# Optimization experiments

Measured on AMD Instinct MI355X. Metric: run time of the kernel, lower is better.

## Reference

```python
import jax, jax.numpy as jnp
import numpy as np

C = 256       # in_channels
IC = 128      # inter_channels = C // 2
G = 4         # num_group
D = IC // G   # per-group channels = 32
B, H, W_ = 4, 56, 56
EPS = 1e-5


def conv1x1(x, w, b=None):
    # x: (B,Cin,H,W), w: (Cout,Cin)
    y = jnp.einsum('bchw,oc->bohw', x, w)
    if b is not None:
        y = y + b[None, :, None, None]
    return y


def bn(x, scale, bias, mean, var):
    inv = scale / jnp.sqrt(var + EPS)
    return x * inv[None, :, None, None] + (bias - mean * inv)[None, :, None, None]


def setup_inputs():
    key = jax.random.key(0)
    ks = jax.random.split(key, 16)
    r = lambda k, shape, s=0.05: jax.random.normal(k, shape, jnp.float32) * s
    C4 = C // 4
    return {
        'x': jax.random.normal(ks[0], (B, C, H, W_), jnp.float32),
        'g_w': r(ks[1], (IC, C)), 'g_b': r(ks[2], (IC,)),
        'theta_w': r(ks[3], (IC, C)), 'theta_b': r(ks[4], (IC,)),
        'phi_w': r(ks[5], (IC, C)), 'phi_b': r(ks[6], (IC,)),
        'W_w': r(ks[7], (C, IC)), 'W_b': r(ks[8], (C,)),
        'bnW_scale': jnp.ones((C,)), 'bnW_bias': jnp.zeros((C,)),
        'bnW_mean': jnp.zeros((C,)), 'bnW_var': jnp.ones((C,)),
        'ff1_w': r(ks[9], (C4, C)),
        'ffbn1_scale': jnp.ones((C4,)), 'ffbn1_bias': jnp.zeros((C4,)),
        'ffbn1_mean': jnp.zeros((C4,)), 'ffbn1_var': jnp.ones((C4,)),
        'ff2_w': r(ks[10], (C4, C4, 3, 3)),
        'ffbn2_scale': jnp.ones((C4,)), 'ffbn2_bias': jnp.zeros((C4,)),
        'ffbn2_mean': jnp.zeros((C4,)), 'ffbn2_var': jnp.ones((C4,)),
        'ff3_w': r(ks[11], (C, C4)),
        'ffbn3_scale': jnp.ones((C,)), 'ffbn3_bias': jnp.zeros((C,)),
        'ffbn3_mean': jnp.zeros((C,)), 'ffbn3_var': jnp.ones((C,)),
    }


def reference(x, g_w, g_b, theta_w, theta_b, phi_w, phi_b, W_w, W_b,
              bnW_scale, bnW_bias, bnW_mean, bnW_var,
              ff1_w, ffbn1_scale, ffbn1_bias, ffbn1_mean, ffbn1_var,
              ff2_w, ffbn2_scale, ffbn2_bias, ffbn2_mean, ffbn2_var,
              ff3_w, ffbn3_scale, ffbn3_bias, ffbn3_mean, ffbn3_var):
    b, c, h, w = x.shape
    n = h * w
    # grouped non-local attention: channels split into G groups of D
    gx = conv1x1(x, g_w, g_b).reshape(b, G, D, n)       # (B,G,D,N)
    tx = conv1x1(x, theta_w, theta_b).reshape(b, G, D, n)
    px = conv1x1(x, phi_w, phi_b).reshape(b, G, D, n)
    f = jnp.einsum('bgdn,bgdm->bgnm', tx, px)           # (B,G,N,N) scores
    attn = jax.nn.softmax(f, axis=-1)                   # softmax over keys (torch dim=2 on (b,N,N))
    yy = jnp.einsum('bgnm,bgdm->bgdn', attn, gx)        # (B,G,D,N)
    y_out = yy.reshape(b, IC, h, w)
    W_y = bn(conv1x1(y_out, W_w, W_b), bnW_scale, bnW_bias, bnW_mean, bnW_var)
    z = jax.nn.relu(W_y + x)
    # FPNFFConv bottleneck FFN (BN in eval mode)
    o = jax.nn.relu(bn(conv1x1(z, ff1_w), ffbn1_scale, ffbn1_bias, ffbn1_mean, ffbn1_var))
    o = jax.lax.conv_general_dilated(o, ff2_w, (1, 1), 'SAME',
                                     dimension_numbers=('NCHW', 'OIHW', 'NCHW'))
    o = jax.nn.relu(bn(o, ffbn2_scale, ffbn2_bias, ffbn2_mean, ffbn2_var))
    o = bn(conv1x1(o, ff3_w), ffbn3_scale, ffbn3_bias, ffbn3_mean, ffbn3_var)
    return jax.nn.relu(o + z)
```

## Files before the change

kernel.cpp:

```cpp
#include <hip/hip_runtime.h>
#include <hip/hip_bf16.h>

#define NPIX 3136
#define BB 4
#define LOG2E 1.4426950408889634f

typedef unsigned short u16;
typedef __bf16 bf16x8 __attribute__((ext_vector_type(8)));
typedef float f32x4 __attribute__((ext_vector_type(4)));

__device__ __forceinline__ float b2f(u16 u) {
  union { unsigned u; float f; } c; c.u = ((unsigned)u) << 16; return c.f;
}
__device__ __forceinline__ u16 f2b(float f) {
  __hip_bfloat16 h = __float2bfloat16(f);
  return *reinterpret_cast<u16*>(&h);
}
__device__ __forceinline__ unsigned pk2(float a, float b) {
  return (unsigned)f2b(a) | ((unsigned)f2b(b) << 16);
}
__device__ __forceinline__ f32x4 mfma(bf16x8 a, bf16x8 b, f32x4 c) {
  return __builtin_amdgcn_mfma_f32_16x16x32_bf16(a, b, c, 0, 0, 0);
}

template<int NSTEP, int NOT>
__device__ __forceinline__ void mf_gemm2(const u16* __restrict__ A0,
                                         const u16* __restrict__ A1,
                                         const u16* __restrict__ Brow, int sB,
                                         int lq, f32x4* acc) {
#pragma unroll
  for (int s = 0; s < NSTEP; ++s) {
    bf16x8 bf[NOT];
#pragma unroll
    for (int ot = 0; ot < NOT; ++ot)
      bf[ot] = *(const bf16x8*)(Brow + (size_t)ot * 16 * sB + s * 32 + lq * 8);
    bf16x8 a0 = *(const bf16x8*)(A0 + s * 32 + lq * 8);
    bf16x8 a1 = *(const bf16x8*)(A1 + s * 32 + lq * 8);
#pragma unroll
    for (int ot = 0; ot < NOT; ++ot) {
      acc[ot] = mfma(a0, bf[ot], acc[ot]);
      acc[NOT + ot] = mfma(a1, bf[ot], acc[NOT + ot]);
    }
  }
}

__global__ __launch_bounds__(256) void prep_w(
    const float* __restrict__ gw, const float* __restrict__ tw,
    const float* __restrict__ pw, const float* __restrict__ Ww,
    const float* __restrict__ f1w, const float* __restrict__ f2w,
    const float* __restrict__ f3w,
    u16* __restrict__ gwb, u16* __restrict__ twb, u16* __restrict__ pwb,
    u16* __restrict__ Wwb, u16* __restrict__ f1b, u16* __restrict__ f3b,
    u16* __restrict__ f2p) {
  for (int i = blockIdx.x * 256 + threadIdx.x; i < 200704; i += gridDim.x * 256) {
    int j = i;
    if (j < 32768) { gwb[j] = f2b(gw[j]); continue; } j -= 32768;
    if (j < 32768) { twb[j] = f2b(tw[j] * LOG2E); continue; } j -= 32768;
    if (j < 32768) { pwb[j] = f2b(pw[j]); continue; } j -= 32768;
    if (j < 32768) { Wwb[j] = f2b(Ww[j]); continue; } j -= 32768;
    if (j < 16384) { f1b[j] = f2b(f1w[j]); continue; } j -= 16384;
    if (j < 16384) { f3b[j] = f2b(f3w[j]); continue; } j -= 16384;
    int t = j >> 12, rem = j & 4095, co = rem >> 6, ci = rem & 63;
    f2p[j] = f2b(f2w[(co * 64 + ci) * 9 + t]);
  }
}

__global__ __launch_bounds__(256) void prep_x(const float* __restrict__ x,
                                              u16* __restrict__ xt) {
  __shared__ u16 sT[64 * 65];
  const int b = blockIdx.z, c0 = blockIdx.y * 64, n0 = blockIdx.x * 64;
  const int t = threadIdx.x;
#pragma unroll
  for (int cc = 0; cc < 4; ++cc) {
    int c = cc * 16 + (t >> 4), n4 = (t & 15) * 4;
    float4 v = *(const float4*)(x + ((size_t)(b * 256 + c0 + c)) * NPIX + n0 + n4);
    sT[c * 65 + n4 + 0] = f2b(v.x);
    sT[c * 65 + n4 + 1] = f2b(v.y);
    sT[c * 65 + n4 + 2] = f2b(v.z);
    sT[c * 65 + n4 + 3] = f2b(v.w);
  }
  __syncthreads();
#pragma unroll
  for (int nn = 0; nn < 4; ++nn) {
    int n = nn * 16 + (t >> 4), c4 = (t & 15) * 4;
    uint2 s;
    s.x = (unsigned)sT[(c4 + 0) * 65 + n] | ((unsigned)sT[(c4 + 1) * 65 + n] << 16);
    s.y = (unsigned)sT[(c4 + 2) * 65 + n] | ((unsigned)sT[(c4 + 3) * 65 + n] << 16);
    *(uint2*)(xt + ((size_t)b * NPIX + n0 + n) * 256 + c0 + c4) = s;
  }
}

__global__ __launch_bounds__(256) void proj_kernel(
    const u16* __restrict__ xt,
    const u16* __restrict__ gwb, const u16* __restrict__ twb, const u16* __restrict__ pwb,
    const float* __restrict__ gb, const float* __restrict__ tb, const float* __restrict__ pb,
    u16* __restrict__ gx, u16* __restrict__ Tq, u16* __restrict__ Pk) {
  const int b = blockIdx.z, oc = blockIdx.y, nb = blockIdx.x * 128;
  const int sec = oc >> 1, rbase = (oc & 1) * 64;
  const u16* wsel = sec == 0 ? gwb : (sec == 1 ? twb : pwb);
  const float* bsel = sec == 0 ? gb : (sec == 1 ? tb : pb);
  const int wv = threadIdx.x >> 6, lane = threadIdx.x & 63;
  const int lr = lane & 15, lq = lane >> 4;
  const int nrow0 = nb + wv * 32, nrow1 = nrow0 + 16;
  const int r0 = nrow0 + lr < NPIX ? nrow0 + lr : NPIX - 1;
  const int r1 = nrow1 + lr < NPIX ? nrow1 + lr : NPIX - 1;
  f32x4 acc[8] = {};
  mf_gemm2<8, 4>(xt + ((size_t)b * NPIX + r0) * 256,
                 xt + ((size_t)b * NPIX + r1) * 256,
                 wsel + (size_t)(rbase + lr) * 256, 256, lq, acc);
#pragma unroll
  for (int t = 0; t < 2; ++t) {
    const int qn = (t ? nrow1 : nrow0) + lq * 4;
    if (qn >= NPIX) continue;
#pragma unroll
    for (int ot = 0; ot < 4; ++ot) {
      const f32x4 a = acc[t * 4 + ot];
      const int o = rbase + ot * 16 + lr;
      float bias = bsel[o];
      if (sec == 1) bias *= LOG2E;
      if (sec == 0) {
        uint2 s;
        s.x = pk2(a[0] + bias, a[1] + bias);
        s.y = pk2(a[2] + bias, a[3] + bias);
        *(uint2*)(gx + ((size_t)b * 128 + o) * NPIX + qn) = s;
      } else {
        const int g = o >> 5, dl = o & 31;
        u16* dst = sec == 1 ? Tq : Pk;
        size_t base = (size_t)(b * 4 + g) * NPIX;
#pragma unroll
        for (int r = 0; r < 4; ++r)
          dst[(base + qn + r) * 32 + dl] = f2b(a[r] + bias);
      }
    }
  }
}

__global__ __launch_bounds__(256) void attn_kernel(
    const u16* __restrict__ Tq, const u16* __restrict__ Pk,
    const u16* __restrict__ gx, u16* __restrict__ OPb, float* __restrict__ LP) {
  __shared__ __align__(16) u16 Plds[4][32][40];
  const int bid = blockIdx.x;
  const int ks = bid / 400, rem = bid % 400;
  const int bg = rem / 25, qblk = rem % 25;
  const int b = bg >> 2, g = bg & 3;
  const int wave = threadIdx.x >> 6, lane = threadIdx.x & 63;
  const int lr = lane & 15, lq = lane >> 4;
  const int qbase = qblk * 128 + wave * 32;
  const int kc0 = ks * 448;
  const u16* Qp = Tq + (size_t)bg * NPIX * 32;
  const u16* Kp = Pk + (size_t)bg * NPIX * 32;
  const u16* Vp = gx + ((size_t)b * 128 + g * 32) * NPIX;

  bf16x8 qf[2];
#pragma unroll
  for (int qi = 0; qi < 2; ++qi) {
    int row = qbase + qi * 16 + lr;
    row = row < NPIX ? row : NPIX - 1;
    qf[qi] = *(const bf16x8*)(Qp + (size_t)row * 32 + lq * 8);
  }
  const f32x4 z4 = {0.f, 0.f, 0.f, 0.f};
  f32x4 O[2][2], Lf[2];
#pragma unroll
  for (int qi = 0; qi < 2; ++qi) { O[qi][0] = z4; O[qi][1] = z4; Lf[qi] = z4; }
  bf16x8 onef;
#pragma unroll
  for (int j = 0; j < 8; ++j) onef[j] = (__bf16)1.0f;

#pragma unroll 1
  for (int kc = kc0; kc < kc0 + 448; kc += 32) {
    bf16x8 kf0 = *(const bf16x8*)(Kp + (size_t)(kc + lr) * 32 + lq * 8);
    bf16x8 kf1 = *(const bf16x8*)(Kp + (size_t)(kc + 16 + lr) * 32 + lq * 8);
    f32x4 S[2][2];
    S[0][0] = mfma(qf[0], kf0, z4);
    S[0][1] = mfma(qf[0], kf1, z4);
    S[1][0] = mfma(qf[1], kf0, z4);
    S[1][1] = mfma(qf[1], kf1, z4);
#pragma unroll
    for (int qi = 0; qi < 2; ++qi)
#pragma unroll
      for (int kt = 0; kt < 2; ++kt)
#pragma unroll
        for (int r = 0; r < 4; ++r) {
          unsigned u = __builtin_bit_cast(unsigned, __builtin_exp2f(S[qi][kt][r]));
          Plds[wave][qi * 16 + lq * 4 + r][kt * 16 + lr] = (u16)(u >> 16);
        }
    bf16x8 pf0 = *(const bf16x8*)(&Plds[wave][lr][lq * 8]);
    bf16x8 pf1 = *(const bf16x8*)(&Plds[wave][16 + lr][lq * 8]);
    bf16x8 vf0 = *(const bf16x8*)(Vp + (size_t)lr * NPIX + kc + lq * 8);
    bf16x8 vf1 = *(const bf16x8*)(Vp + (size_t)(16 + lr) * NPIX + kc + lq * 8);
    O[0][0] = mfma(pf0, vf0, O[0][0]);
    O[0][1] = mfma(pf0, vf1, O[0][1]);
    O[1][0] = mfma(pf1, vf0, O[1][0]);
    O[1][1] = mfma(pf1, vf1, O[1][1]);
    Lf[0] = mfma(pf0, onef, Lf[0]);
    Lf[1] = mfma(pf1, onef, Lf[1]);
  }
  const size_t sbase = (size_t)(ks * 16 + bg) * NPIX;
#pragma unroll
  for (int qi = 0; qi < 2; ++qi) {
#pragma unroll
    for (int r = 0; r < 4; ++r) {
      int qrow = qbase + qi * 16 + lq * 4 + r;
      if (qrow < NPIX) {
        size_t ob = (sbase + qrow) * 32;
        OPb[ob + lr] = f2b(O[qi][0][r]);
        OPb[ob + 16 + lr] = f2b(O[qi][1][r]);
        if (lr == 0) LP[sbase + qrow] = Lf[qi][r];
      }
    }
  }
}

__global__ __launch_bounds__(256) void combine_kernel(
    const u16* __restrict__ OPb, const float* __restrict__ LP,
    u16* __restrict__ yt) {
  const int bg = blockIdx.y, b = bg >> 2, g = bg & 3;
  const int t = threadIdx.x;
  const int n = blockIdx.x * 64 + (t >> 2);
  const int dseg = (t & 3) * 8;
  float a[8] = {};
  float l = 0.f;
#pragma unroll
  for (int ks = 0; ks < 7; ++ks) {
    const u16* src = OPb + ((size_t)(ks * 16 + bg) * NPIX + n) * 32 + dseg;
    uint4 v = *(const uint4*)src;
    const unsigned* vp = (const unsigned*)&v;
#pragma unroll
    for (int k = 0; k < 4; ++k) {
      a[2 * k] += b2f((u16)vp[k]);
      a[2 * k + 1] += b2f((u16)(vp[k] >> 16));
    }
    l += LP[(size_t)(ks * 16 + bg) * NPIX + n];
  }
  float inv = 1.0f / l;
  uint4 s;
  s.x = pk2(a[0] * inv, a[1] * inv);
  s.y = pk2(a[2] * inv, a[3] * inv);
  s.z = pk2(a[4] * inv, a[5] * inv);
  s.w = pk2(a[6] * inv, a[7] * inv);
  *(uint4*)(yt + ((size_t)b * NPIX + n) * 128 + g * 32 + dseg) = s;
}

__global__ __launch_bounds__(256) void wz_kernel(
    const u16* __restrict__ yt, const u16* __restrict__ Wwb, const float* __restrict__ Wb,
    const float* __restrict__ sc, const float* __restrict__ bi,
    const float* __restrict__ mu, const float* __restrict__ var,
    const float* __restrict__ x, u16* __restrict__ zt) {
  const int b = blockIdx.z, oc = blockIdx.y, nb = blockIdx.x * 128;
  const int wv = threadIdx.x >> 6, lane = threadIdx.x & 63;
  const int lr = lane & 15, lq = lane >> 4;
  const int nrow0 = nb + wv * 32, nrow1 = nrow0 + 16;
  const int r0 = nrow0 + lr < NPIX ? nrow0 + lr : NPIX - 1;
  const int r1 = nrow1 + lr < NPIX ? nrow1 + lr : NPIX - 1;
  f32x4 acc[8] = {};
  mf_gemm2<4, 4>(yt + ((size_t)b * NPIX + r0) * 128,
                 yt + ((size_t)b * NPIX + r1) * 128,
                 Wwb + (size_t)(oc * 64 + lr) * 128, 128, lq, acc);
#pragma unroll
  for (int t = 0; t < 2; ++t) {
    const int qn = (t ? nrow1 : nrow0) + lq * 4;
    if (qn >= NPIX) continue;
#pragma unroll
    for (int ot = 0; ot < 4; ++ot) {
      const f32x4 a = acc[t * 4 + ot];
      const int o = oc * 64 + ot * 16 + lr;
      float inv = sc[o] * rsqrtf(var[o] + 1e-5f);
      float off = bi[o] - mu[o] * inv + Wb[o] * inv;
      float4 xr = *(const float4*)(x + ((size_t)b * 256 + o) * NPIX + qn);
      float xv[4] = {xr.x, xr.y, xr.z, xr.w};
#pragma unroll
      for (int r = 0; r < 4; ++r) {
        float v = fmaxf(a[r] * inv + off + xv[r], 0.f);
        zt[((size_t)b * NPIX + qn + r) * 256 + o] = f2b(v);
      }
    }
  }
}

__global__ __launch_bounds__(256) void ff1_kernel(
    const u16* __restrict__ zt, const u16* __restrict__ f1b,
    const float* __restrict__ sc, const float* __restrict__ bi,
    const float* __restrict__ mu, const float* __restrict__ var,
    u16* __restrict__ o1t) {
  const int b = blockIdx.z, oc = blockIdx.y, nb = blockIdx.x * 128;
  const int wv = threadIdx.x >> 6, lane = threadIdx.x & 63;
  const int lr = lane & 15, lq = lane >> 4;
  const int nrow0 = nb + wv * 32, nrow1 = nrow0 + 16;
  const int r0 = nrow0 + lr < NPIX ? nrow0 + lr : NPIX - 1;
  const int r1 = nrow1 + lr < NPIX ? nrow1 + lr : NPIX - 1;
  f32x4 acc[4] = {};
  mf_gemm2<8, 2>(zt + ((size_t)b * NPIX + r0) * 256,
                 zt + ((size_t)b * NPIX + r1) * 256,
                 f1b + (size_t)(oc * 32 + lr) * 256, 256, lq, acc);
#pragma unroll
  for (int t = 0; t < 2; ++t) {
    const int qn = (t ? nrow1 : nrow0) + lq * 4;
    if (qn >= NPIX) continue;
#pragma unroll
    for (int ot = 0; ot < 2; ++ot) {
      const f32x4 a = acc[t * 2 + ot];
      const int o = oc * 32 + ot * 16 + lr;
      float inv = sc[o] * rsqrtf(var[o] + 1e-5f);
      float off = bi[o] - mu[o] * inv;
#pragma unroll
      for (int r = 0; r < 4; ++r) {
        float v = fmaxf(a[r] * inv + off, 0.f);
        o1t[((size_t)b * NPIX + qn + r) * 64 + o] = f2b(v);
      }
    }
  }
}

__global__ __launch_bounds__(256) void ff2_kernel(
    const u16* __restrict__ o1t, const u16* __restrict__ f2p,
    const float* __restrict__ sc, const float* __restrict__ bi,
    const float* __restrict__ mu, const float* __restrict__ var,
    u16* __restrict__ o2t) {
  const int b = blockIdx.z, oc = blockIdx.y, nb = blockIdx.x * 128;
  const int wv = threadIdx.x >> 6, lane = threadIdx.x & 63;
  const int lr = lane & 15, lq = lane >> 4;
  const int n0 = nb + wv * 32 + lr, n1 = n0 + 16;
  const int h0 = n0 / 56, w0 = n0 % 56;
  const int h1 = n1 / 56, w1 = n1 % 56;
  f32x4 acc[4] = {};
#pragma unroll
  for (int t = 0; t < 9; ++t) {
    const int dh = t / 3 - 1, dw = t % 3 - 1;
    const bool v0 = (h0 + dh) >= 0 && (h0 + dh) < 56 && (w0 + dw) >= 0 && (w0 + dw) < 56;
    const bool v1 = (h1 + dh) >= 0 && (h1 + dh) < 56 && (w1 + dw) >= 0 && (w1 + dw) < 56;
    const u16* A0 = o1t + ((size_t)b * NPIX + n0 + dh * 56 + dw) * 64;
    const u16* A1 = o1t + ((size_t)b * NPIX + n1 + dh * 56 + dw) * 64;
    const u16* Br = f2p + (size_t)t * 4096 + (size_t)(oc * 32 + lr) * 64;
#pragma unroll
    for (int k2 = 0; k2 < 2; ++k2) {
      bf16x8 bf0 = *(const bf16x8*)(Br + k2 * 32 + lq * 8);
      bf16x8 bf1 = *(const bf16x8*)(Br + (size_t)16 * 64 + k2 * 32 + lq * 8);
      bf16x8 a0 = {}, a1 = {};
      if (v0) a0 = *(const bf16x8*)(A0 + k2 * 32 + lq * 8);
      if (v1) a1 = *(const bf16x8*)(A1 + k2 * 32 + lq * 8);
      acc[0] = mfma(a0, bf0, acc[0]);
      acc[1] = mfma(a0, bf1, acc[1]);
      acc[2] = mfma(a1, bf0, acc[2]);
      acc[3] = mfma(a1, bf1, acc[3]);
    }
  }
  const int nrow0 = nb + wv * 32;
#pragma unroll
  for (int t = 0; t < 2; ++t) {
    const int qn = nrow0 + t * 16 + lq * 4;
    if (qn >= NPIX) continue;
#pragma unroll
    for (int ot = 0; ot < 2; ++ot) {
      const f32x4 a = acc[t * 2 + ot];
      const int o = oc * 32 + ot * 16 + lr;
      float inv = sc[o] * rsqrtf(var[o] + 1e-5f);
      float off = bi[o] - mu[o] * inv;
#pragma unroll
      for (int r = 0; r < 4; ++r) {
        float v = fmaxf(a[r] * inv + off, 0.f);
        o2t[((size_t)b * NPIX + qn + r) * 64 + o] = f2b(v);
      }
    }
  }
}

__global__ __launch_bounds__(256) void ff3_kernel(
    const u16* __restrict__ o2t, const u16* __restrict__ f3b,
    const float* __restrict__ sc, const float* __restrict__ bi,
    const float* __restrict__ mu, const float* __restrict__ var,
    const u16* __restrict__ zt, float* __restrict__ out) {
  const int b = blockIdx.z, oc = blockIdx.y, nb = blockIdx.x * 128;
  const int wv = threadIdx.x >> 6, lane = threadIdx.x & 63;
  const int lr = lane & 15, lq = lane >> 4;
  const int nrow0 = nb + wv * 32, nrow1 = nrow0 + 16;
  const int r0 = nrow0 + lr < NPIX ? nrow0 + lr : NPIX - 1;
  const int r1 = nrow1 + lr < NPIX ? nrow1 + lr : NPIX - 1;
  f32x4 acc[8] = {};
  mf_gemm2<2, 4>(o2t + ((size_t)b * NPIX + r0) * 64,
                 o2t + ((size_t)b * NPIX + r1) * 64,
                 f3b + (size_t)(oc * 64 + lr) * 64, 64, lq, acc);
#pragma unroll
  for (int t = 0; t < 2; ++t) {
    const int qn = (t ? nrow1 : nrow0) + lq * 4;
    if (qn >= NPIX) continue;
#pragma unroll
    for (int ot = 0; ot < 4; ++ot) {
      const f32x4 a = acc[t * 4 + ot];
      const int o = oc * 64 + ot * 16 + lr;
      float inv = sc[o] * rsqrtf(var[o] + 1e-5f);
      float off = bi[o] - mu[o] * inv;
      float4 s;
      float* sv = (float*)&s;
#pragma unroll
      for (int r = 0; r < 4; ++r) {
        float zres = b2f(zt[((size_t)b * NPIX + qn + r) * 256 + o]);
        sv[r] = fmaxf(a[r] * inv + off + zres, 0.f);
      }
      *(float4*)(out + ((size_t)b * 256 + o) * NPIX + qn) = s;
    }
  }
}

extern "C" void kernel_launch(void* const* d_in, const int* in_sizes, int n_in,
                              void* d_out, int out_size, void* d_ws, size_t ws_size,
                              hipStream_t stream) {
  const float* x    = (const float*)d_in[0];
  const float* gw   = (const float*)d_in[1];
  const float* gb   = (const float*)d_in[2];
  const float* tw   = (const float*)d_in[3];
  const float* tb   = (const float*)d_in[4];
  const float* pw   = (const float*)d_in[5];
  const float* pb   = (const float*)d_in[6];
  const float* Ww   = (const float*)d_in[7];
  const float* Wb   = (const float*)d_in[8];
  const float* bnWs = (const float*)d_in[9];
  const float* bnWb = (const float*)d_in[10];
  const float* bnWm = (const float*)d_in[11];
  const float* bnWv = (const float*)d_in[12];
  const float* f1w  = (const float*)d_in[13];
  const float* b1s  = (const float*)d_in[14];
  const float* b1b  = (const float*)d_in[15];
  const float* b1m  = (const float*)d_in[16];
  const float* b1v  = (const float*)d_in[17];
  const float* f2w  = (const float*)d_in[18];
  const float* b2s  = (const float*)d_in[19];
  const float* b2b  = (const float*)d_in[20];
  const float* b2m  = (const float*)d_in[21];
  const float* b2v  = (const float*)d_in[22];
  const float* f3w  = (const float*)d_in[23];
  const float* b3s  = (const float*)d_in[24];
  const float* b3b  = (const float*)d_in[25];
  const float* b3m  = (const float*)d_in[26];
  const float* b3v  = (const float*)d_in[27];
  float* out = (float*)d_out;

  u16* p = (u16*)d_ws;
  u16* xt  = p; p += (size_t)BB * NPIX * 256;
  u16* gwb = p; p += 128 * 256;
  u16* twb = p; p += 128 * 256;
  u16* pwb = p; p += 128 * 256;
  u16* Wwb = p; p += 256 * 128;
  u16* f1b = p; p += 64 * 256;
  u16* f3b = p; p += 256 * 64;
  u16* f2p = p; p += 9 * 64 * 64;
  u16* Tq  = p; p += (size_t)16 * NPIX * 32;
  u16* Pk  = p; p += (size_t)16 * NPIX * 32;
  u16* gx  = p; p += (size_t)BB * 128 * NPIX;
  u16* yt  = p; p += (size_t)BB * NPIX * 128;
  u16* OPb = p; p += (size_t)7 * 16 * NPIX * 32;
  float* LP = (float*)p; p += (size_t)7 * 16 * NPIX * 2;
  u16* zt  = p; p += (size_t)BB * NPIX * 256;
  u16* o1t = p; p += (size_t)BB * NPIX * 64;
  u16* o2t = p; p += (size_t)BB * NPIX * 64;

  prep_w<<<dim3(196), 256, 0, stream>>>(gw, tw, pw, Ww, f1w, f2w, f3w,
                                        gwb, twb, pwb, Wwb, f1b, f3b, f2p);
  prep_x<<<dim3(49, 4, BB), 256, 0, stream>>>(x, xt);
  proj_kernel<<<dim3(25, 6, BB), 256, 0, stream>>>(xt, gwb, twb, pwb, gb, tb, pb,
                                                   gx, Tq, Pk);
  attn_kernel<<<dim3(2800), 256, 0, stream>>>(Tq, Pk, gx, OPb, LP);
  combine_kernel<<<dim3(49, 16), 256, 0, stream>>>(OPb, LP, yt);
  wz_kernel<<<dim3(25, 4, BB), 256, 0, stream>>>(yt, Wwb, Wb, bnWs, bnWb, bnWm, bnWv,
                                                 x, zt);
  ff1_kernel<<<dim3(25, 2, BB), 256, 0, stream>>>(zt, f1b, b1s, b1b, b1m, b1v, o1t);
  ff2_kernel<<<dim3(25, 2, BB), 256, 0, stream>>>(o1t, f2p, b2s, b2b, b2m, b2v, o2t);
  ff3_kernel<<<dim3(25, 4, BB), 256, 0, stream>>>(o2t, f3b, b3s, b3b, b3m, b3v, zt, out);
}
```

Before: 250.9 us.

## Fuse x transpose into projection and split-K combine into W conv

```diff
diff --git a/kernel.cpp b/kernel.cpp
--- a/kernel.cpp
+++ b/kernel.cpp
@@ -65,71 +65,62 @@
   }
 }
 
-__global__ __launch_bounds__(256) void prep_x(const float* __restrict__ x,
-                                              u16* __restrict__ xt) {
-  __shared__ u16 sT[64 * 65];
-  const int b = blockIdx.z, c0 = blockIdx.y * 64, n0 = blockIdx.x * 64;
-  const int t = threadIdx.x;
-#pragma unroll
-  for (int cc = 0; cc < 4; ++cc) {
-    int c = cc * 16 + (t >> 4), n4 = (t & 15) * 4;
-    float4 v = *(const float4*)(x + ((size_t)(b * 256 + c0 + c)) * NPIX + n0 + n4);
-    sT[c * 65 + n4 + 0] = f2b(v.x);
-    sT[c * 65 + n4 + 1] = f2b(v.y);
-    sT[c * 65 + n4 + 2] = f2b(v.z);
-    sT[c * 65 + n4 + 3] = f2b(v.w);
-  }
-  __syncthreads();
-#pragma unroll
-  for (int nn = 0; nn < 4; ++nn) {
-    int n = nn * 16 + (t >> 4), c4 = (t & 15) * 4;
-    uint2 s;
-    s.x = (unsigned)sT[(c4 + 0) * 65 + n] | ((unsigned)sT[(c4 + 1) * 65 + n] << 16);
-    s.y = (unsigned)sT[(c4 + 2) * 65 + n] | ((unsigned)sT[(c4 + 3) * 65 + n] << 16);
-    *(uint2*)(xt + ((size_t)b * NPIX + n0 + n) * 256 + c0 + c4) = s;
-  }
-}
-
 __global__ __launch_bounds__(256) void proj_kernel(
-    const u16* __restrict__ xt,
+    const float* __restrict__ x,
     const u16* __restrict__ gwb, const u16* __restrict__ twb, const u16* __restrict__ pwb,
     const float* __restrict__ gb, const float* __restrict__ tb, const float* __restrict__ pb,
     u16* __restrict__ gx, u16* __restrict__ Tq, u16* __restrict__ Pk) {
-  const int b = blockIdx.z, oc = blockIdx.y, nb = blockIdx.x * 128;
-  const int sec = oc >> 1, rbase = (oc & 1) * 64;
-  const u16* wsel = sec == 0 ? gwb : (sec == 1 ? twb : pwb);
-  const float* bsel = sec == 0 ? gb : (sec == 1 ? tb : pb);
-  const int wv = threadIdx.x >> 6, lane = threadIdx.x & 63;
-  const int lr = lane & 15, lq = lane >> 4;
-  const int nrow0 = nb + wv * 32, nrow1 = nrow0 + 16;
-  const int r0 = nrow0 + lr < NPIX ? nrow0 + lr : NPIX - 1;
-  const int r1 = nrow1 + lr < NPIX ? nrow1 + lr : NPIX - 1;
-  f32x4 acc[8] = {};
-  mf_gemm2<8, 4>(xt + ((size_t)b * NPIX + r0) * 256,
-                 xt + ((size_t)b * NPIX + r1) * 256,
-                 wsel + (size_t)(rbase + lr) * 256, 256, lq, acc);
-#pragma unroll
-  for (int t = 0; t < 2; ++t) {
-    const int qn = (t ? nrow1 : nrow0) + lq * 4;
-    if (qn >= NPIX) continue;
+  __shared__ __align__(16) u16 sA[64 * 264];
+  const int b = blockIdx.y, nb = blockIdx.x * 64;
+  const int tid = threadIdx.x;
+  const int cb16 = tid >> 4, jj = tid & 15;
+#pragma unroll 4
+  for (int cb = 0; cb < 16; ++cb) {
+    int c = cb * 16 + cb16;
+    float4 v = *(const float4*)(x + ((size_t)(b * 256 + c)) * NPIX + nb + jj * 4);
+    int n0 = jj * 4;
+    sA[(n0 + 0) * 264 + c] = f2b(v.x);
+    sA[(n0 + 1) * 264 + c] = f2b(v.y);
+    sA[(n0 + 2) * 264 + c] = f2b(v.z);
+    sA[(n0 + 3) * 264 + c] = f2b(v.w);
+  }
+  __syncthreads();
+  const int wv = tid >> 6, lane = tid & 63;
+  const int lr = lane & 15, lq = lane >> 4;
+  const int nrow = nb + wv * 16;
+#pragma unroll 1
+  for (int sec = 0; sec < 6; ++sec) {
+    const int st = sec >> 1, rbase = (sec & 1) * 64;
+    const u16* wsel = st == 0 ? gwb : (st == 1 ? twb : pwb);
+    const float* bsel = st == 0 ? gb : (st == 1 ? tb : pb);
+    f32x4 acc[4] = {};
+#pragma unroll
+    for (int s = 0; s < 8; ++s) {
+      bf16x8 af = *(const bf16x8*)(sA + (wv * 16 + lr) * 264 + s * 32 + lq * 8);
+#pragma unroll
+      for (int ot = 0; ot < 4; ++ot) {
+        bf16x8 bf = *(const bf16x8*)(wsel + (size_t)(rbase + ot * 16 + lr) * 256 + s * 32 + lq * 8);
+        acc[ot] = mfma(af, bf, acc[ot]);
+      }
+    }
+    const int qn = nrow + lq * 4;
 #pragma unroll
     for (int ot = 0; ot < 4; ++ot) {
-      const f32x4 a = acc[t * 4 + ot];
       const int o = rbase + ot * 16 + lr;
       float bias = bsel[o];
-      if (sec == 1) bias *= LOG2E;
-      if (sec == 0) {
-        uint2 s;
-        s.x = pk2(a[0] + bias, a[1] + bias);
-        s.y = pk2(a[2] + bias, a[3] + bias);
-        *(uint2*)(gx + ((size_t)b * 128 + o) * NPIX + qn) = s;
+      if (st == 1) bias *= LOG2E;
+      if (st == 0) {
+        uint2 s2;
+        s2.x = pk2(acc[ot][0] + bias, acc[ot][1] + bias);
+        s2.y = pk2(acc[ot][2] + bias, acc[ot][3] + bias);
+        *(uint2*)(gx + ((size_t)b * 128 + o) * NPIX + qn) = s2;
       } else {
         const int g = o >> 5, dl = o & 31;
-        u16* dst = sec == 1 ? Tq : Pk;
+        u16* dst = st == 1 ? Tq : Pk;
         size_t base = (size_t)(b * 4 + g) * NPIX;
 #pragma unroll
         for (int r = 0; r < 4; ++r)
-          dst[(base + qn + r) * 32 + dl] = f2b(a[r] + bias);
+          dst[(base + qn + r) * 32 + dl] = f2b(acc[ot][r] + bias);
       }
     }
   }
@@ -211,68 +202,58 @@
   }
 }
 
-__global__ __launch_bounds__(256) void combine_kernel(
+__global__ __launch_bounds__(256) void wz_kernel(
     const u16* __restrict__ OPb, const float* __restrict__ LP,
-    u16* __restrict__ yt) {
-  const int bg = blockIdx.y, b = bg >> 2, g = bg & 3;
-  const int t = threadIdx.x;
-  const int n = blockIdx.x * 64 + (t >> 2);
-  const int dseg = (t & 3) * 8;
-  float a[8] = {};
-  float l = 0.f;
-#pragma unroll
-  for (int ks = 0; ks < 7; ++ks) {
-    const u16* src = OPb + ((size_t)(ks * 16 + bg) * NPIX + n) * 32 + dseg;
-    uint4 v = *(const uint4*)src;
-    const unsigned* vp = (const unsigned*)&v;
-#pragma unroll
-    for (int k = 0; k < 4; ++k) {
-      a[2 * k] += b2f((u16)vp[k]);
-      a[2 * k + 1] += b2f((u16)(vp[k] >> 16));
-    }
-    l += LP[(size_t)(ks * 16 + bg) * NPIX + n];
-  }
-  float inv = 1.0f / l;
-  uint4 s;
-  s.x = pk2(a[0] * inv, a[1] * inv);
-  s.y = pk2(a[2] * inv, a[3] * inv);
-  s.z = pk2(a[4] * inv, a[5] * inv);
-  s.w = pk2(a[6] * inv, a[7] * inv);
-  *(uint4*)(yt + ((size_t)b * NPIX + n) * 128 + g * 32 + dseg) = s;
-}
-
-__global__ __launch_bounds__(256) void wz_kernel(
-    const u16* __restrict__ yt, const u16* __restrict__ Wwb, const float* __restrict__ Wb,
+    const u16* __restrict__ Wwb, const float* __restrict__ Wb,
     const float* __restrict__ sc, const float* __restrict__ bi,
     const float* __restrict__ mu, const float* __restrict__ var,
     const float* __restrict__ x, u16* __restrict__ zt) {
-  const int b = blockIdx.z, oc = blockIdx.y, nb = blockIdx.x * 128;
-  const int wv = threadIdx.x >> 6, lane = threadIdx.x & 63;
-  const int lr = lane & 15, lq = lane >> 4;
-  const int nrow0 = nb + wv * 32, nrow1 = nrow0 + 16;
-  const int r0 = nrow0 + lr < NPIX ? nrow0 + lr : NPIX - 1;
-  const int r1 = nrow1 + lr < NPIX ? nrow1 + lr : NPIX - 1;
-  f32x4 acc[8] = {};
-  mf_gemm2<4, 4>(yt + ((size_t)b * NPIX + r0) * 128,
-                 yt + ((size_t)b * NPIX + r1) * 128,
-                 Wwb + (size_t)(oc * 64 + lr) * 128, 128, lq, acc);
-#pragma unroll
-  for (int t = 0; t < 2; ++t) {
-    const int qn = (t ? nrow1 : nrow0) + lq * 4;
-    if (qn >= NPIX) continue;
-#pragma unroll
-    for (int ot = 0; ot < 4; ++ot) {
-      const f32x4 a = acc[t * 4 + ot];
-      const int o = oc * 64 + ot * 16 + lr;
-      float inv = sc[o] * rsqrtf(var[o] + 1e-5f);
-      float off = bi[o] - mu[o] * inv + Wb[o] * inv;
-      float4 xr = *(const float4*)(x + ((size_t)b * 256 + o) * NPIX + qn);
-      float xv[4] = {xr.x, xr.y, xr.z, xr.w};
-#pragma unroll
-      for (int r = 0; r < 4; ++r) {
-        float v = fmaxf(a[r] * inv + off + xv[r], 0.f);
-        zt[((size_t)b * NPIX + qn + r) * 256 + o] = f2b(v);
-      }
+  __shared__ float Ls[4][64];
+  const int b = blockIdx.z, oc = blockIdx.y, nb = blockIdx.x * 64;
+  const int tid = threadIdx.x;
+  {
+    int g = tid >> 6, row = tid & 63;
+    float l = 0.f;
+#pragma unroll
+    for (int ks = 0; ks < 7; ++ks)
+      l += LP[(size_t)(ks * 16 + b * 4 + g) * NPIX + nb + row];
+    Ls[g][row] = 1.0f / l;
+  }
+  __syncthreads();
+  const int wv = tid >> 6, lane = tid & 63;
+  const int lr = lane & 15, lq = lane >> 4;
+  const int nrow = nb + wv * 16;
+  f32x4 acc[4][4] = {};
+#pragma unroll
+  for (int g = 0; g < 4; ++g) {
+    bf16x8 bf[4];
+#pragma unroll
+    for (int ot = 0; ot < 4; ++ot)
+      bf[ot] = *(const bf16x8*)(Wwb + (size_t)(oc * 64 + ot * 16 + lr) * 128 + g * 32 + lq * 8);
+#pragma unroll
+    for (int ks = 0; ks < 7; ++ks) {
+      bf16x8 af = *(const bf16x8*)(OPb +
+          ((size_t)(ks * 16 + b * 4 + g) * NPIX + nrow + lr) * 32 + lq * 8);
+#pragma unroll
+      for (int ot = 0; ot < 4; ++ot)
+        acc[g][ot] = mfma(af, bf[ot], acc[g][ot]);
+    }
+  }
+#pragma unroll
+  for (int ot = 0; ot < 4; ++ot) {
+    const int o = oc * 64 + ot * 16 + lr;
+    float inv = sc[o] * rsqrtf(var[o] + 1e-5f);
+    float off = bi[o] - mu[o] * inv + Wb[o] * inv;
+    const int qn = nrow + lq * 4;
+    float4 xr = *(const float4*)(x + ((size_t)b * 256 + o) * NPIX + qn);
+    float xv[4] = {xr.x, xr.y, xr.z, xr.w};
+#pragma unroll
+    for (int r = 0; r < 4; ++r) {
+      int row = wv * 16 + lq * 4 + r;
+      float y = acc[0][ot][r] * Ls[0][row] + acc[1][ot][r] * Ls[1][row] +
+                acc[2][ot][r] * Ls[2][row] + acc[3][ot][r] * Ls[3][row];
+      float v = fmaxf(y * inv + off + xv[r], 0.f);
+      zt[((size_t)b * NPIX + qn + r) * 256 + o] = f2b(v);
     }
   }
 }
@@ -435,7 +416,6 @@
   float* out = (float*)d_out;
 
   u16* p = (u16*)d_ws;
-  u16* xt  = p; p += (size_t)BB * NPIX * 256;
   u16* gwb = p; p += 128 * 256;
   u16* twb = p; p += 128 * 256;
   u16* pwb = p; p += 128 * 256;
@@ -446,7 +426,6 @@
   u16* Tq  = p; p += (size_t)16 * NPIX * 32;
   u16* Pk  = p; p += (size_t)16 * NPIX * 32;
   u16* gx  = p; p += (size_t)BB * 128 * NPIX;
-  u16* yt  = p; p += (size_t)BB * NPIX * 128;
   u16* OPb = p; p += (size_t)7 * 16 * NPIX * 32;
   float* LP = (float*)p; p += (size_t)7 * 16 * NPIX * 2;
   u16* zt  = p; p += (size_t)BB * NPIX * 256;
@@ -455,13 +434,11 @@
 
   prep_w<<<dim3(196), 256, 0, stream>>>(gw, tw, pw, Ww, f1w, f2w, f3w,
                                         gwb, twb, pwb, Wwb, f1b, f3b, f2p);
-  prep_x<<<dim3(49, 4, BB), 256, 0, stream>>>(x, xt);
-  proj_kernel<<<dim3(25, 6, BB), 256, 0, stream>>>(xt, gwb, twb, pwb, gb, tb, pb,
-                                                   gx, Tq, Pk);
+  proj_kernel<<<dim3(49, BB), 256, 0, stream>>>(x, gwb, twb, pwb, gb, tb, pb,
+                                                gx, Tq, Pk);
   attn_kernel<<<dim3(2800), 256, 0, stream>>>(Tq, Pk, gx, OPb, LP);
-  combine_kernel<<<dim3(49, 16), 256, 0, stream>>>(OPb, LP, yt);
-  wz_kernel<<<dim3(25, 4, BB), 256, 0, stream>>>(yt, Wwb, Wb, bnWs, bnWb, bnWm, bnWv,
-                                                 x, zt);
+  wz_kernel<<<dim3(49, 4, BB), 256, 0, stream>>>(OPb, LP, Wwb, Wb,
+                                                 bnWs, bnWb, bnWm, bnWv, x, zt);
   ff1_kernel<<<dim3(25, 2, BB), 256, 0, stream>>>(zt, f1b, b1s, b1b, b1m, b1v, o1t);
   ff2_kernel<<<dim3(25, 2, BB), 256, 0, stream>>>(o1t, f2p, b2s, b2b, b2m, b2v, o2t);
   ff3_kernel<<<dim3(25, 4, BB), 256, 0, stream>>>(o2t, f3b, b3s, b3b, b3m, b3v, zt, out);
```

Measured after the change: 275.5 us. 1.1x slower.

## Fuse split-K attention combine into W projection kernel

Applied to the files above, without the earlier changes.

```diff
diff --git a/kernel.cpp b/kernel.cpp
--- a/kernel.cpp
+++ b/kernel.cpp
@@ -211,68 +211,59 @@
   }
 }
 
-__global__ __launch_bounds__(256) void combine_kernel(
+__global__ __launch_bounds__(512) void wz_kernel(
     const u16* __restrict__ OPb, const float* __restrict__ LP,
-    u16* __restrict__ yt) {
-  const int bg = blockIdx.y, b = bg >> 2, g = bg & 3;
-  const int t = threadIdx.x;
-  const int n = blockIdx.x * 64 + (t >> 2);
-  const int dseg = (t & 3) * 8;
-  float a[8] = {};
-  float l = 0.f;
-#pragma unroll
-  for (int ks = 0; ks < 7; ++ks) {
-    const u16* src = OPb + ((size_t)(ks * 16 + bg) * NPIX + n) * 32 + dseg;
-    uint4 v = *(const uint4*)src;
-    const unsigned* vp = (const unsigned*)&v;
-#pragma unroll
-    for (int k = 0; k < 4; ++k) {
-      a[2 * k] += b2f((u16)vp[k]);
-      a[2 * k + 1] += b2f((u16)(vp[k] >> 16));
-    }
-    l += LP[(size_t)(ks * 16 + bg) * NPIX + n];
-  }
-  float inv = 1.0f / l;
-  uint4 s;
-  s.x = pk2(a[0] * inv, a[1] * inv);
-  s.y = pk2(a[2] * inv, a[3] * inv);
-  s.z = pk2(a[4] * inv, a[5] * inv);
-  s.w = pk2(a[6] * inv, a[7] * inv);
-  *(uint4*)(yt + ((size_t)b * NPIX + n) * 128 + g * 32 + dseg) = s;
-}
-
-__global__ __launch_bounds__(256) void wz_kernel(
-    const u16* __restrict__ yt, const u16* __restrict__ Wwb, const float* __restrict__ Wb,
+    const u16* __restrict__ Wwb, const float* __restrict__ Wb,
     const float* __restrict__ sc, const float* __restrict__ bi,
     const float* __restrict__ mu, const float* __restrict__ var,
     const float* __restrict__ x, u16* __restrict__ zt) {
-  const int b = blockIdx.z, oc = blockIdx.y, nb = blockIdx.x * 128;
-  const int wv = threadIdx.x >> 6, lane = threadIdx.x & 63;
-  const int lr = lane & 15, lq = lane >> 4;
-  const int nrow0 = nb + wv * 32, nrow1 = nrow0 + 16;
-  const int r0 = nrow0 + lr < NPIX ? nrow0 + lr : NPIX - 1;
-  const int r1 = nrow1 + lr < NPIX ? nrow1 + lr : NPIX - 1;
-  f32x4 acc[8] = {};
-  mf_gemm2<4, 4>(yt + ((size_t)b * NPIX + r0) * 128,
-                 yt + ((size_t)b * NPIX + r1) * 128,
-                 Wwb + (size_t)(oc * 64 + lr) * 128, 128, lq, acc);
-#pragma unroll
-  for (int t = 0; t < 2; ++t) {
-    const int qn = (t ? nrow1 : nrow0) + lq * 4;
-    if (qn >= NPIX) continue;
-#pragma unroll
-    for (int ot = 0; ot < 4; ++ot) {
-      const f32x4 a = acc[t * 4 + ot];
-      const int o = oc * 64 + ot * 16 + lr;
-      float inv = sc[o] * rsqrtf(var[o] + 1e-5f);
-      float off = bi[o] - mu[o] * inv + Wb[o] * inv;
-      float4 xr = *(const float4*)(x + ((size_t)b * 256 + o) * NPIX + qn);
-      float xv[4] = {xr.x, xr.y, xr.z, xr.w};
-#pragma unroll
-      for (int r = 0; r < 4; ++r) {
-        float v = fmaxf(a[r] * inv + off + xv[r], 0.f);
-        zt[((size_t)b * NPIX + qn + r) * 256 + o] = f2b(v);
-      }
+  __shared__ float Ls[4][32];
+  const int b = blockIdx.y, nb = blockIdx.x * 32;
+  const int tid = threadIdx.x;
+  if (tid < 128) {
+    int g = tid >> 5, row = tid & 31;
+    float l = 0.f;
+#pragma unroll
+    for (int ks = 0; ks < 7; ++ks)
+      l += LP[(size_t)(ks * 16 + b * 4 + g) * NPIX + nb + row];
+    Ls[g][row] = 1.0f / l;
+  }
+  __syncthreads();
+  const int wave = tid >> 6, lane = tid & 63;
+  const int lr = lane & 15, lq = lane >> 4;
+  const int oc = wave & 3, tt = wave >> 2;
+  const int nrow = nb + tt * 16;
+  f32x4 acc[4][4] = {};
+#pragma unroll
+  for (int g = 0; g < 4; ++g) {
+    bf16x8 bf[4];
+#pragma unroll
+    for (int ot = 0; ot < 4; ++ot)
+      bf[ot] = *(const bf16x8*)(Wwb + (size_t)(oc * 64 + ot * 16 + lr) * 128 + g * 32 + lq * 8);
+#pragma unroll
+    for (int ks = 0; ks < 7; ++ks) {
+      bf16x8 af = *(const bf16x8*)(OPb +
+          ((size_t)(ks * 16 + b * 4 + g) * NPIX + nrow + lr) * 32 + lq * 8);
+#pragma unroll
+      for (int ot = 0; ot < 4; ++ot)
+        acc[g][ot] = mfma(af, bf[ot], acc[g][ot]);
+    }
+  }
+#pragma unroll
+  for (int ot = 0; ot < 4; ++ot) {
+    const int o = oc * 64 + ot * 16 + lr;
+    float inv = sc[o] * rsqrtf(var[o] + 1e-5f);
+    float off = bi[o] - mu[o] * inv + Wb[o] * inv;
+    const int qn = nrow + lq * 4;
+    float4 xr = *(const float4*)(x + ((size_t)b * 256 + o) * NPIX + qn);
+    float xv[4] = {xr.x, xr.y, xr.z, xr.w};
+#pragma unroll
+    for (int r = 0; r < 4; ++r) {
+      int row = tt * 16 + lq * 4 + r;
+      float y = acc[0][ot][r] * Ls[0][row] + acc[1][ot][r] * Ls[1][row] +
+                acc[2][ot][r] * Ls[2][row] + acc[3][ot][r] * Ls[3][row];
+      float v = fmaxf(y * inv + off + xv[r], 0.f);
+      zt[((size_t)b * NPIX + qn + r) * 256 + o] = f2b(v);
     }
   }
 }
@@ -446,7 +437,6 @@
   u16* Tq  = p; p += (size_t)16 * NPIX * 32;
   u16* Pk  = p; p += (size_t)16 * NPIX * 32;
   u16* gx  = p; p += (size_t)BB * 128 * NPIX;
-  u16* yt  = p; p += (size_t)BB * NPIX * 128;
   u16* OPb = p; p += (size_t)7 * 16 * NPIX * 32;
   float* LP = (float*)p; p += (size_t)7 * 16 * NPIX * 2;
   u16* zt  = p; p += (size_t)BB * NPIX * 256;
@@ -459,9 +449,8 @@
   proj_kernel<<<dim3(25, 6, BB), 256, 0, stream>>>(xt, gwb, twb, pwb, gb, tb, pb,
                                                    gx, Tq, Pk);
   attn_kernel<<<dim3(2800), 256, 0, stream>>>(Tq, Pk, gx, OPb, LP);
-  combine_kernel<<<dim3(49, 16), 256, 0, stream>>>(OPb, LP, yt);
-  wz_kernel<<<dim3(25, 4, BB), 256, 0, stream>>>(yt, Wwb, Wb, bnWs, bnWb, bnWm, bnWv,
-                                                 x, zt);
+  wz_kernel<<<dim3(98, BB), 512, 0, stream>>>(OPb, LP, Wwb, Wb,
+                                              bnWs, bnWb, bnWm, bnWv, x, zt);
   ff1_kernel<<<dim3(25, 2, BB), 256, 0, stream>>>(zt, f1b, b1s, b1b, b1m, b1v, o1t);
   ff2_kernel<<<dim3(25, 2, BB), 256, 0, stream>>>(o1t, f2p, b2s, b2b, b2m, b2v, o2t);
   ff3_kernel<<<dim3(25, 4, BB), 256, 0, stream>>>(o2t, f3b, b3s, b3b, b3m, b3v, zt, out);
```

Measured after the change: 248.9 us. About the same (-0.8%).
